# Performance work log

Hardware: AMD Instinct MI355X
Metric: run time of the kernel (lower is better)

The kernel has to match this reference:

```python
import jax, jax.numpy as jnp
import numpy as np

D_MODEL, D_QKV, N_HEADS = 1024, 64, 16


def setup_inputs() -> dict:
    key = jax.random.key(0)
    k_x, k_qkv, k_out = jax.random.split(key, 3)
    X = jax.random.normal(k_x, (2, 2048, D_MODEL), dtype=jnp.float32)
    # nn.Linear(d_model, 3*d_qkv*n_heads, bias=False): store as (in, out) for X @ W
    W_qkv = jax.random.normal(k_qkv, (D_MODEL, 3 * D_QKV * N_HEADS), dtype=jnp.float32) * (D_MODEL ** -0.5)
    W_out = jax.random.normal(k_out, (D_QKV * N_HEADS, D_MODEL), dtype=jnp.float32) * ((D_QKV * N_HEADS) ** -0.5)
    return {"X": X, "W_qkv": W_qkv, "W_out": W_out}


def reference(X, W_qkv, W_out):
    b, s, _ = X.shape
    h, d = N_HEADS, D_QKV
    scale = d ** 0.5
    qkv = X @ W_qkv                          # [b, s, 3*h*d]
    # Faithful to torch: view(b, s, h, d, 3).unbind(-1) -> interleaved q/k/v layout
    qkv = qkv.reshape(b, s, h, d, 3)
    q, k, v = qkv[..., 0], qkv[..., 1], qkv[..., 2]   # each [b, s, h, d]
    scores = jnp.einsum("bqhd,bkhd->bhqk", q, k) / scale
    weights = jax.nn.softmax(scores, axis=-1)          # [b, h, s, s]
    attn = jnp.einsum("bhqk,bkhd->bqhd", weights, v)   # [b, s, h, d]
    return attn.reshape(b, s, h * d) @ W_out           # [b, s, d_model]
```

## Files before the change

### kernel.cpp

```cpp
#include <hip/hip_runtime.h>
#include <hip/hip_bf16.h>
#include <math.h>

typedef __bf16 bf16;
typedef __bf16 bf16x2 __attribute__((ext_vector_type(2)));
typedef __bf16 bf16x4 __attribute__((ext_vector_type(4)));
typedef __bf16 bf16x8 __attribute__((ext_vector_type(8)));
typedef float f32x4 __attribute__((ext_vector_type(4)));
typedef float f32x16 __attribute__((ext_vector_type(16)));
typedef int i32x2 __attribute__((ext_vector_type(2)));
typedef int i32x4 __attribute__((ext_vector_type(4)));

#define MFMA16(a, b, c) __builtin_amdgcn_mfma_f32_16x16x32_bf16(a, b, c, 0, 0, 0)
#define MFMA32(a, b, c) __builtin_amdgcn_mfma_f32_32x32x16_bf16(a, b, c, 0, 0, 0)

constexpr int D_MODEL = 1024;
constexpr int N_QKV   = 3072;
constexpr int BATCH   = 2;
constexpr int SEQ     = 2048;
constexpr int NH      = 16;
constexpr int DH      = 64;
constexpr int M_TOT   = BATCH * SEQ;

__device__ __forceinline__ void gl_lds16(const bf16* g, bf16* l) {
    __builtin_amdgcn_global_load_lds(
        (const __attribute__((address_space(1))) void*)g,
        (__attribute__((address_space(3))) void*)l, 16, 0, 0);
}

__device__ __forceinline__ void pl32swap(int& a, int& b) {
    i32x2 r = __builtin_amdgcn_permlane32_swap(a, b, false, false);
    a = r[0];
    b = r[1];
}

template <int N> __device__ __forceinline__ void waitv() {
    asm volatile("s_waitcnt vmcnt(%0)" :: "n"(N) : "memory");
}
__device__ __forceinline__ void waitlgkm0() {
    asm volatile("s_waitcnt lgkmcnt(0)" ::: "memory");
}

__device__ __forceinline__ void transpose_tile(
    const float* __restrict__ in, bf16* __restrict__ out,
    int K, int N, int n0, int k0, bf16 (*T)[72], bool permute)
{
    const int tid = threadIdx.x;
    const int r   = tid >> 2;
    const int c4  = (tid & 3) * 16;

    const float* src = in + (size_t)(k0 + r) * N + n0 + c4;
    f32x4 v0 = *(const f32x4*)(src + 0);
    f32x4 v1 = *(const f32x4*)(src + 4);
    f32x4 v2 = *(const f32x4*)(src + 8);
    f32x4 v3 = *(const f32x4*)(src + 12);
    #pragma unroll
    for (int j = 0; j < 4; j++) {
        T[c4 + j][r]      = (bf16)v0[j];
        T[c4 + 4 + j][r]  = (bf16)v1[j];
        T[c4 + 8 + j][r]  = (bf16)v2[j];
        T[c4 + 12 + j][r] = (bf16)v3[j];
    }
    __syncthreads();
    int rowg = n0 + r;
    if (permute) {
        const int which = rowg % 3;
        const int h     = rowg / 192;
        const int d     = (rowg % 192) / 3;
        rowg = which * 1024 + h * 64 + d;
    }
    bf16* dst = out + (size_t)rowg * K + k0 + c4;
    *(bf16x8*)(dst)     = *(const bf16x8*)&T[r][c4];
    *(bf16x8*)(dst + 8) = *(const bf16x8*)&T[r][c4 + 8];
}

__global__ __launch_bounds__(256) void prepass_kernel(
    const float* __restrict__ X, const float* __restrict__ Wqkv,
    const float* __restrict__ Wout,
    bf16* __restrict__ xb, bf16* __restrict__ wqkv_t, bf16* __restrict__ wout_t)
{
    __shared__ bf16 T[64][72];
    const int b = blockIdx.x;
    if (b < 2048) {
        const size_t i = ((size_t)b * 256 + threadIdx.x) * 8;
        f32x4 a0 = *(const f32x4*)(X + i);
        f32x4 a1 = *(const f32x4*)(X + i + 4);
        bf16x8 w;
        #pragma unroll
        for (int j = 0; j < 4; j++) { w[j] = (bf16)a0[j]; w[j + 4] = (bf16)a1[j]; }
        *(bf16x8*)(xb + i) = w;
    } else if (b < 2048 + 768) {
        const int idx = b - 2048;
        transpose_tile(Wqkv, wqkv_t, D_MODEL, N_QKV,
                       (idx % 48) * 64, (idx / 48) * 64, T, true);
    } else {
        const int idx = b - 2816;
        transpose_tile(Wout, wout_t, D_MODEL, D_MODEL,
                       (idx % 16) * 64, (idx / 16) * 64, T, false);
    }
}

__global__ __launch_bounds__(512, 2) void qkv_gemm_kernel(
    const bf16* __restrict__ Xb, const bf16* __restrict__ Wt,
    bf16* __restrict__ qb, bf16* __restrict__ kb, bf16* __restrict__ vb)
{
    __shared__ __align__(16) bf16 smem[65536];
    bf16* const sA = smem;
    bf16* const sB = smem + 32768;

    const int tid  = threadIdx.x;
    const int wave = tid >> 6;
    const int lane = tid & 63;
    const int quad = lane >> 4;
    const int l16  = lane & 15;
    const int wr   = wave >> 2;
    const int wc   = wave & 3;
    const int m0   = blockIdx.x * 256;
    const int n0   = blockIdx.y * 256;

    const int sr2  = tid >> 3;
    const int c8p  = (tid & 7) ^ (sr2 & 7);
    const int stR0 = (sr2 << 1) | (c8p >> 2);
    const int stC0 = (c8p & 3) << 3;

    const bf16* Asrc = Xb + (size_t)(m0 + stR0) * D_MODEL + stC0;
    const bf16* Bsrc = Wt + (size_t)(n0 + stR0) * D_MODEL + stC0;

#define STG(s, kbo)                                                          \
    do {                                                                     \
        gl_lds16(Asrc + (kbo),                 sA + (s) * 8192 + tid * 8);   \
        gl_lds16(Asrc + 128 * D_MODEL + (kbo), sA + (s) * 8192 + 4096 + tid * 8); \
        gl_lds16(Bsrc + (kbo),                 sB + (s) * 8192 + tid * 8);   \
        gl_lds16(Bsrc + 128 * D_MODEL + (kbo), sB + (s) * 8192 + 4096 + tid * 8); \
    } while (0)

    const int foff = ((l16 >> 1) << 6) +
                     (((((l16 & 1) << 2) | quad) ^ ((l16 >> 1) & 7)) << 3);

    f32x4 acc[8][4];
    #pragma unroll
    for (int a = 0; a < 8; a++)
        #pragma unroll
        for (int b = 0; b < 4; b++) acc[a][b] = {0.f, 0.f, 0.f, 0.f};

#define PHASE(s, jn, DOSTG, WV)                                              \
    {                                                                        \
        const bf16* Ab_ = sA + (s) * 8192 + wr * 4096;                       \
        const bf16* Bb_ = sB + (s) * 8192 + wc * 2048;                       \
        bf16x8 af[8], bfr[4];                                                \
        _Pragma("unroll") for (int mi = 0; mi < 8; mi++)                     \
            af[mi] = *(const bf16x8*)&Ab_[mi * 512 + foff];                  \
        _Pragma("unroll") for (int ni = 0; ni < 4; ni++)                     \
            bfr[ni] = *(const bf16x8*)&Bb_[ni * 512 + foff];                 \
        waitlgkm0();                                                         \
        __builtin_amdgcn_s_barrier();                                        \
        if (DOSTG) { STG((s), (jn) * 32); }                                  \
        __builtin_amdgcn_s_setprio(1);                                       \
        _Pragma("unroll") for (int mi = 0; mi < 8; mi++)                     \
            _Pragma("unroll") for (int ni = 0; ni < 4; ni++)                 \
                acc[mi][ni] = MFMA16(af[mi], bfr[ni], acc[mi][ni]);          \
        __builtin_amdgcn_s_setprio(0);                                       \
        waitv<WV>();                                                         \
        __builtin_amdgcn_s_barrier();                                        \
    }

    STG(0, 0); STG(1, 32); STG(2, 64); STG(3, 96);
    waitv<12>();
    __builtin_amdgcn_s_barrier();

    for (int t = 0; t < 7; ++t) {
        const int j = t * 4;
        PHASE(0, j + 4, true, 12)
        PHASE(1, j + 5, true, 12)
        PHASE(2, j + 6, true, 12)
        PHASE(3, j + 7, true, 12)
    }
    PHASE(0, 0, false, 8)
    PHASE(1, 0, false, 4)
    PHASE(2, 0, false, 0)
    PHASE(3, 0, false, 0)

#undef PHASE
#undef STG

    const int bb     = m0 >> 11;
    const int s_base = m0 & (SEQ - 1);

    if (n0 < 2048) {
        bf16* dst0 = (n0 < 1024) ? qb : kb;
        const int h = ((n0 + wc * 64) >> 6) & 15;
        const size_t bh = (size_t)(bb * NH + h);
        #pragma unroll
        for (int mi = 0; mi < 8; mi++) {
            const int s0 = s_base + wr * 128 + mi * 16 + quad * 4;
            #pragma unroll
            for (int ni = 0; ni < 4; ni++) {
                const int d = ni * 16 + l16;
                #pragma unroll
                for (int i = 0; i < 4; i++)
                    dst0[(bh * SEQ + s0 + i) * DH + d] = (bf16)acc[mi][ni][i];
            }
        }
    } else {
        __syncthreads();
        bf16* T = smem;
        #pragma unroll
        for (int ni = 0; ni < 4; ni++) {
            const int nl = wc * 64 + ni * 16 + l16;
            #pragma unroll
            for (int mi = 0; mi < 8; mi++) {
                const int ml = wr * 128 + mi * 16 + quad * 4;
                bf16x4 pv;
                #pragma unroll
                for (int i = 0; i < 4; i++) pv[i] = (bf16)acc[mi][ni][i];
                const int c   = ml >> 3;
                const int swz = (c & 24) | ((c ^ nl) & 7);
                *(bf16x4*)&T[nl * 256 + swz * 8 + (ml & 7)] = pv;
            }
        }
        __syncthreads();
        const int hbase = (n0 - 2048) >> 6;
        #pragma unroll
        for (int it = 0; it < 8; it++) {
            const int nl = (tid >> 4) + it * 32;
            const int h  = hbase + (nl >> 6);
            const int d  = nl & 63;
            const size_t obase = ((size_t)(bb * NH + h) * DH + d) * SEQ + s_base;
            #pragma unroll
            for (int cc = 0; cc < 2; cc++) {
                const int c   = (tid & 15) + cc * 16;
                const int swz = (c & 24) | ((c ^ nl) & 7);
                bf16x8 vv = *(const bf16x8*)&T[nl * 256 + swz * 8];
                *(bf16x8*)(vb + obase + c * 8) = vv;
            }
        }
    }
}

__global__ __launch_bounds__(512, 4) void attn_kernel(
    const bf16* __restrict__ qb, const bf16* __restrict__ kb,
    const bf16* __restrict__ vb, bf16* __restrict__ ob)
{
    __shared__ __align__(16) bf16 smem[32768];

    const int tid  = threadIdx.x;
    const int wave = tid >> 6;
    const int grp  = wave >> 2;
    const int wq   = wave & 3;
    const int lane = tid & 63;
    const int l32  = lane & 31;
    const int hi   = lane >> 5;
    const int ltid = tid & 255;
    const int bh   = blockIdx.x;
    const int q0   = blockIdx.y * 128;
    const size_t base  = (size_t)bh * SEQ * DH;
    const int    kbase = grp * (SEQ / 2);

    bf16* const KsB = smem + grp * 2 * 4096;
    bf16* const VtB = smem + 16384 + grp * 2 * 4096;

    constexpr float QSCALE = 0.125f * 1.44269504f;

    bf16x8 qf[4];
    {
        const size_t qoff = base + (size_t)(q0 + wq * 32 + l32) * DH + hi * 8;
        #pragma unroll
        for (int kc = 0; kc < 4; kc++) {
            qf[kc] = *(const bf16x8*)(qb + qoff + kc * 16);
            #pragma unroll
            for (int j = 0; j < 8; j++)
                qf[kc][j] = (bf16)((float)qf[kc][j] * QSCALE);
        }
    }

    f32x16 o_acc[2];
    #pragma unroll
    for (int i = 0; i < 16; i++) { o_acc[0][i] = 0.f; o_acc[1][i] = 0.f; }
    float l_acc = 0.f;

    const int so0 = ltid;
    const int so1 = 256 + ltid;
    const int sr0 = so0 >> 3, sc0 = ((so0 & 7) ^ (sr0 & 7)) * 8;
    const int sr1 = so1 >> 3, sc1 = ((so1 & 7) ^ (sr1 & 7)) * 8;

    #define STAGE(bufi, kk0)                                                   \
        do {                                                                   \
            gl_lds16(kb + base + (size_t)(kbase + (kk0) + sr0) * DH + sc0,     \
                     KsB + (bufi) * 4096 + so0 * 8);                           \
            gl_lds16(kb + base + (size_t)(kbase + (kk0) + sr1) * DH + sc1,     \
                     KsB + (bufi) * 4096 + so1 * 8);                           \
            gl_lds16(vb + base + (size_t)sr0 * SEQ + kbase + (kk0) + sc0,      \
                     VtB + (bufi) * 4096 + so0 * 8);                           \
            gl_lds16(vb + base + (size_t)sr1 * SEQ + kbase + (kk0) + sc1,      \
                     VtB + (bufi) * 4096 + so1 * 8);                           \
        } while (0)

    STAGE(0, 0);
    int buf = 0;

    for (int kt = 0; kt < SEQ / 128; ++kt) {
        __syncthreads();
        if (kt + 1 < SEQ / 128) STAGE(buf ^ 1, (kt + 1) * 64);

        const bf16* Kst = KsB + buf * 4096;
        const bf16* Vtt = VtB + buf * 4096;

        #pragma unroll
        for (int kblk = 0; kblk < 2; kblk++) {
            f32x16 sacc;
            #pragma unroll
            for (int i = 0; i < 16; i++) sacc[i] = 0.f;
            #pragma unroll
            for (int kc = 0; kc < 4; kc++) {
                const int cko = ((2 * kc + hi) ^ (l32 & 7)) * 8;
                bf16x8 kf = *(const bf16x8*)
                    &Kst[(kblk * 32 + l32) * 64 + cko];
                sacc = MFMA32(kf, qf[kc], sacc);
            }

            int w[8];
            #pragma unroll
            for (int c = 0; c < 8; c++) {
                const float e0 = __builtin_amdgcn_exp2f(sacc[2 * c]);
                const float e1 = __builtin_amdgcn_exp2f(sacc[2 * c + 1]);
                l_acc += e0;
                l_acc += e1;
                bf16x2 t; t[0] = (bf16)e0; t[1] = (bf16)e1;
                w[c] = __builtin_bit_cast(int, t);
            }
            #pragma unroll
            for (int cc = 0; cc < 2; cc++) {
                pl32swap(w[cc * 4 + 0], w[cc * 4 + 2]);
                pl32swap(w[cc * 4 + 1], w[cc * 4 + 3]);
                i32x4 fi = {w[cc * 4 + 0], w[cc * 4 + 1],
                            w[cc * 4 + 2], w[cc * 4 + 3]};
                bf16x8 pa = __builtin_bit_cast(bf16x8, fi);

                const int kc = kblk * 2 + cc;
                const int cko = ((2 * kc + hi) ^ (l32 & 7)) * 8;
                #pragma unroll
                for (int nb = 0; nb < 2; nb++) {
                    bf16x8 vf = *(const bf16x8*)
                        &Vtt[(nb * 32 + l32) * 64 + cko];
                    o_acc[nb] = MFMA32(pa, vf, o_acc[nb]);
                }
            }
        }
        buf ^= 1;
    }
    #undef STAGE

    const float l_q = l_acc + __shfl_xor(l_acc, 32);

    float* cO  = (float*)smem;
    float* cL1 = (float*)smem + 8192;
    float* cL2 = (float*)smem + 8320;

    __syncthreads();
    if (grp == 1) {
        #pragma unroll
        for (int nb = 0; nb < 2; nb++)
            #pragma unroll
            for (int c4 = 0; c4 < 4; c4++) {
                const int j = nb * 4 + c4;
                f32x4 v = { o_acc[nb][c4 * 4 + 0], o_acc[nb][c4 * 4 + 1],
                            o_acc[nb][c4 * 4 + 2], o_acc[nb][c4 * 4 + 3] };
                *(f32x4*)&cO[(wq * 64 + lane) * 32 + ((j ^ (lane & 7)) * 4)] = v;
            }
        if (hi == 0) cL1[wq * 32 + l32] = l_q;
    }
    __syncthreads();
    if (grp == 0) {
        #pragma unroll
        for (int nb = 0; nb < 2; nb++)
            #pragma unroll
            for (int c4 = 0; c4 < 4; c4++) {
                const int j = nb * 4 + c4;
                f32x4 v = *(const f32x4*)
                    &cO[(wq * 64 + lane) * 32 + ((j ^ (lane & 7)) * 4)];
                #pragma unroll
                for (int e = 0; e < 4; e++) o_acc[nb][c4 * 4 + e] += v[e];
            }
        if (hi == 0) cL2[wq * 32 + l32] = l_q + cL1[wq * 32 + l32];
    }
    __syncthreads();
    if (grp == 0) {
        const int b = bh >> 4, h = bh & 15;
        #pragma unroll
        for (int i = 0; i < 16; i++) {
            const int qrow = (i & 3) + 8 * (i >> 2) + 4 * hi;
            const int q = q0 + wq * 32 + qrow;
            const float li = 1.0f / cL2[wq * 32 + qrow];
            #pragma unroll
            for (int nb = 0; nb < 2; nb++)
                ob[((size_t)(b * SEQ + q) * NH + h) * DH + nb * 32 + l32] =
                    (bf16)(o_acc[nb][i] * li);
        }
    }
}

__global__ __launch_bounds__(256) void out_gemm_kernel(
    const bf16* __restrict__ A, const bf16* __restrict__ Wt,
    float* __restrict__ out)
{
    __shared__ __align__(16) bf16 As[128 * 64];
    __shared__ __align__(16) bf16 Bs[128 * 64];

    const int tid  = threadIdx.x;
    const int wave = tid >> 6;
    const int lane = tid & 63;
    const int quad = lane >> 4;
    const int l16  = lane & 15;
    const int sw   = l16 & 7;
    const int m0   = blockIdx.x * 128;
    const int n0   = blockIdx.y * 128;
    const int wm   = (wave & 1) * 64;
    const int wn   = (wave >> 1) * 64;

    const int srow = lane >> 3;
    const int sc_s = ((lane & 7) ^ srow) * 8;
    const int sc_d = (lane & 7) * 8;

    f32x4 acc[4][4];
    #pragma unroll
    for (int a = 0; a < 4; a++)
        #pragma unroll
        for (int b = 0; b < 4; b++) acc[a][b] = {0.f, 0.f, 0.f, 0.f};

    for (int kb0 = 0; kb0 < D_MODEL; kb0 += 64) {
        __syncthreads();
        #pragma unroll
        for (int j = 0; j < 4; j++) {
            const int row = wave * 32 + j * 8 + srow;
            gl_lds16(A  + (size_t)(m0 + row) * D_MODEL + kb0 + sc_s,
                     As + row * 64 + sc_d);
            gl_lds16(Wt + (size_t)(n0 + row) * D_MODEL + kb0 + sc_s,
                     Bs + row * 64 + sc_d);
        }
        __syncthreads();

        #pragma unroll
        for (int ks = 0; ks < 2; ks++) {
            const int co = ((ks * 4 + quad) ^ sw) * 8;
            bf16x8 af[4], bfr[4];
            #pragma unroll
            for (int mi = 0; mi < 4; mi++)
                af[mi] = *(const bf16x8*)&As[(wm + mi * 16 + l16) * 64 + co];
            #pragma unroll
            for (int ni = 0; ni < 4; ni++)
                bfr[ni] = *(const bf16x8*)&Bs[(wn + ni * 16 + l16) * 64 + co];
            #pragma unroll
            for (int mi = 0; mi < 4; mi++)
                #pragma unroll
                for (int ni = 0; ni < 4; ni++)
                    acc[mi][ni] = MFMA16(af[mi], bfr[ni], acc[mi][ni]);
        }
    }

    #pragma unroll
    for (int mi = 0; mi < 4; mi++) {
        const int row0 = m0 + wm + mi * 16 + quad * 4;
        #pragma unroll
        for (int ni = 0; ni < 4; ni++) {
            const int n = n0 + wn + ni * 16 + l16;
            #pragma unroll
            for (int i = 0; i < 4; i++)
                out[(size_t)(row0 + i) * D_MODEL + n] = acc[mi][ni][i];
        }
    }
}

extern "C" void kernel_launch(void* const* d_in, const int* in_sizes, int n_in,
                              void* d_out, int out_size, void* d_ws, size_t ws_size,
                              hipStream_t stream)
{
    const float* X    = (const float*)d_in[0];
    const float* Wqkv = (const float*)d_in[1];
    const float* Wout = (const float*)d_in[2];
    float* out        = (float*)d_out;

    const size_t n_elem = (size_t)M_TOT * D_MODEL;
    bf16* qb      = (bf16*)d_ws;
    bf16* kb      = qb + n_elem;
    bf16* vb      = kb + n_elem;
    bf16* attnb   = vb + n_elem;
    bf16* wqkv_t  = attnb + n_elem;
    bf16* wout_t  = wqkv_t + (size_t)N_QKV * D_MODEL;
    bf16* xb      = wout_t + (size_t)D_MODEL * D_MODEL;

    prepass_kernel<<<3072, 256, 0, stream>>>(X, Wqkv, Wout, xb, wqkv_t, wout_t);

    qkv_gemm_kernel<<<dim3(M_TOT / 256, N_QKV / 256), 512, 0, stream>>>(
        xb, wqkv_t, qb, kb, vb);
    attn_kernel<<<dim3(BATCH * NH, SEQ / 128), 512, 0, stream>>>(qb, kb, vb, attnb);
    out_gemm_kernel<<<dim3(M_TOT / 128, D_MODEL / 128), 256, 0, stream>>>(
        attnb, wout_t, out);
}
```

Measured before the change: 176.7 us.

## Pipeline out-projection GEMM with 4-stage LDS ring and compute row sums via MFMA

The output-projection GEMM is rebuilt around a four-stage LDS ring buffer with k-chunks of 32. Loads are issued asynchronously ahead of compute, fenced by explicit waitcnt and barrier calls, with raised wave priority around the MFMAs, so global-load latency overlaps with matrix math instead of sitting behind two syncthreads per iteration. In the attention kernel the softmax denominator is now accumulated by an extra MFMA against a vector of ones instead of scalar adds. This removes the per-element adds and one reduction barrier, but the sum is taken over bf16-rounded weights, which changes numerics slightly. The GEMM adds launch_bounds(256,2) and doubles its shared memory to 64KB.

```diff
diff --git a/kernel.cpp b/kernel.cpp
--- a/kernel.cpp
+++ b/kernel.cpp
@@ -273,10 +273,16 @@
         }
     }
 
+    bf16x8 ones;
+    #pragma unroll
+    for (int j = 0; j < 8; j++) ones[j] = (bf16)1.0f;
+
     f32x16 o_acc[2];
+    f32x16 o_l;
     #pragma unroll
-    for (int i = 0; i < 16; i++) { o_acc[0][i] = 0.f; o_acc[1][i] = 0.f; }
-    float l_acc = 0.f;
+    for (int i = 0; i < 16; i++) {
+        o_acc[0][i] = 0.f; o_acc[1][i] = 0.f; o_l[i] = 0.f;
+    }
 
     const int so0 = ltid;
     const int so1 = 256 + ltid;
@@ -321,11 +327,9 @@
             int w[8];
             #pragma unroll
             for (int c = 0; c < 8; c++) {
-                const float e0 = __builtin_amdgcn_exp2f(sacc[2 * c]);
-                const float e1 = __builtin_amdgcn_exp2f(sacc[2 * c + 1]);
-                l_acc += e0;
-                l_acc += e1;
-                bf16x2 t; t[0] = (bf16)e0; t[1] = (bf16)e1;
+                bf16x2 t;
+                t[0] = (bf16)__builtin_amdgcn_exp2f(sacc[2 * c]);
+                t[1] = (bf16)__builtin_amdgcn_exp2f(sacc[2 * c + 1]);
                 w[c] = __builtin_bit_cast(int, t);
             }
             #pragma unroll
@@ -338,6 +342,7 @@
 
                 const int kc = kblk * 2 + cc;
                 const int cko = ((2 * kc + hi) ^ (l32 & 7)) * 8;
+                o_l = MFMA32(pa, ones, o_l);
                 #pragma unroll
                 for (int nb = 0; nb < 2; nb++) {
                     bf16x8 vf = *(const bf16x8*)
@@ -350,11 +355,8 @@
     }
     #undef STAGE
 
-    const float l_q = l_acc + __shfl_xor(l_acc, 32);
-
     float* cO  = (float*)smem;
     float* cL1 = (float*)smem + 8192;
-    float* cL2 = (float*)smem + 8320;
 
     __syncthreads();
     if (grp == 1) {
@@ -367,7 +369,11 @@
                             o_acc[nb][c4 * 4 + 2], o_acc[nb][c4 * 4 + 3] };
                 *(f32x4*)&cO[(wq * 64 + lane) * 32 + ((j ^ (lane & 7)) * 4)] = v;
             }
-        if (hi == 0) cL1[wq * 32 + l32] = l_q;
+        if (l32 == 0) {
+            #pragma unroll
+            for (int i = 0; i < 16; i++)
+                cL1[wq * 32 + ((i & 3) + 8 * (i >> 2) + 4 * hi)] = o_l[i];
+        }
     }
     __syncthreads();
     if (grp == 0) {
@@ -381,16 +387,12 @@
                 #pragma unroll
                 for (int e = 0; e < 4; e++) o_acc[nb][c4 * 4 + e] += v[e];
             }
-        if (hi == 0) cL2[wq * 32 + l32] = l_q + cL1[wq * 32 + l32];
-    }
-    __syncthreads();
-    if (grp == 0) {
         const int b = bh >> 4, h = bh & 15;
         #pragma unroll
         for (int i = 0; i < 16; i++) {
             const int qrow = (i & 3) + 8 * (i >> 2) + 4 * hi;
             const int q = q0 + wq * 32 + qrow;
-            const float li = 1.0f / cL2[wq * 32 + qrow];
+            const float li = 1.0f / (o_l[i] + cL1[wq * 32 + qrow]);
             #pragma unroll
             for (int nb = 0; nb < 2; nb++)
                 ob[((size_t)(b * SEQ + q) * NH + h) * DH + nb * 32 + l32] =
@@ -399,27 +401,42 @@
     }
 }
 
-__global__ __launch_bounds__(256) void out_gemm_kernel(
+__global__ __launch_bounds__(256, 2) void out_gemm_kernel(
     const bf16* __restrict__ A, const bf16* __restrict__ Wt,
     float* __restrict__ out)
 {
-    __shared__ __align__(16) bf16 As[128 * 64];
-    __shared__ __align__(16) bf16 Bs[128 * 64];
+    __shared__ __align__(16) bf16 smem[32768];
+    bf16* const sA = smem;
+    bf16* const sB = smem + 16384;
 
     const int tid  = threadIdx.x;
     const int wave = tid >> 6;
     const int lane = tid & 63;
     const int quad = lane >> 4;
     const int l16  = lane & 15;
-    const int sw   = l16 & 7;
+    const int wr   = wave >> 1;
+    const int wc   = wave & 1;
     const int m0   = blockIdx.x * 128;
     const int n0   = blockIdx.y * 128;
-    const int wm   = (wave & 1) * 64;
-    const int wn   = (wave >> 1) * 64;
-
-    const int srow = lane >> 3;
-    const int sc_s = ((lane & 7) ^ srow) * 8;
-    const int sc_d = (lane & 7) * 8;
+
+    const int sr2  = tid >> 3;
+    const int c8p  = (tid & 7) ^ (sr2 & 7);
+    const int stR0 = (sr2 << 1) | (c8p >> 2);
+    const int stC0 = (c8p & 3) << 3;
+
+    const bf16* Asrc = A  + (size_t)(m0 + stR0) * D_MODEL + stC0;
+    const bf16* Bsrc = Wt + (size_t)(n0 + stR0) * D_MODEL + stC0;
+
+#define STG(s, kbo)                                                          \
+    do {                                                                     \
+        gl_lds16(Asrc + (kbo),                sA + (s) * 4096 + tid * 8);    \
+        gl_lds16(Asrc + 64 * D_MODEL + (kbo), sA + (s) * 4096 + 2048 + tid * 8); \
+        gl_lds16(Bsrc + (kbo),                sB + (s) * 4096 + tid * 8);    \
+        gl_lds16(Bsrc + 64 * D_MODEL + (kbo), sB + (s) * 4096 + 2048 + tid * 8); \
+    } while (0)
+
+    const int foff = ((l16 >> 1) << 6) +
+                     (((((l16 & 1) << 2) | quad) ^ ((l16 >> 1) & 7)) << 3);
 
     f32x4 acc[4][4];
     #pragma unroll
@@ -427,42 +444,52 @@
         #pragma unroll
         for (int b = 0; b < 4; b++) acc[a][b] = {0.f, 0.f, 0.f, 0.f};
 
-    for (int kb0 = 0; kb0 < D_MODEL; kb0 += 64) {
-        __syncthreads();
-        #pragma unroll
-        for (int j = 0; j < 4; j++) {
-            const int row = wave * 32 + j * 8 + srow;
-            gl_lds16(A  + (size_t)(m0 + row) * D_MODEL + kb0 + sc_s,
-                     As + row * 64 + sc_d);
-            gl_lds16(Wt + (size_t)(n0 + row) * D_MODEL + kb0 + sc_s,
-                     Bs + row * 64 + sc_d);
-        }
-        __syncthreads();
-
-        #pragma unroll
-        for (int ks = 0; ks < 2; ks++) {
-            const int co = ((ks * 4 + quad) ^ sw) * 8;
-            bf16x8 af[4], bfr[4];
-            #pragma unroll
-            for (int mi = 0; mi < 4; mi++)
-                af[mi] = *(const bf16x8*)&As[(wm + mi * 16 + l16) * 64 + co];
-            #pragma unroll
-            for (int ni = 0; ni < 4; ni++)
-                bfr[ni] = *(const bf16x8*)&Bs[(wn + ni * 16 + l16) * 64 + co];
-            #pragma unroll
-            for (int mi = 0; mi < 4; mi++)
-                #pragma unroll
-                for (int ni = 0; ni < 4; ni++)
-                    acc[mi][ni] = MFMA16(af[mi], bfr[ni], acc[mi][ni]);
-        }
-    }
+#define PHASE(s, jn, DOSTG, WV)                                              \
+    {                                                                        \
+        const bf16* Ab_ = sA + (s) * 4096 + wr * 2048;                       \
+        const bf16* Bb_ = sB + (s) * 4096 + wc * 2048;                       \
+        bf16x8 af[4], bfr[4];                                                \
+        _Pragma("unroll") for (int mi = 0; mi < 4; mi++)                     \
+            af[mi] = *(const bf16x8*)&Ab_[mi * 512 + foff];                  \
+        _Pragma("unroll") for (int ni = 0; ni < 4; ni++)                     \
+            bfr[ni] = *(const bf16x8*)&Bb_[ni * 512 + foff];                 \
+        waitlgkm0();                                                         \
+        __builtin_amdgcn_s_barrier();                                        \
+        if (DOSTG) { STG((s), (jn) * 32); }                                  \
+        __builtin_amdgcn_s_setprio(1);                                       \
+        _Pragma("unroll") for (int mi = 0; mi < 4; mi++)                     \
+            _Pragma("unroll") for (int ni = 0; ni < 4; ni++)                 \
+                acc[mi][ni] = MFMA16(af[mi], bfr[ni], acc[mi][ni]);          \
+        __builtin_amdgcn_s_setprio(0);                                       \
+        waitv<WV>();                                                         \
+        __builtin_amdgcn_s_barrier();                                        \
+    }
+
+    STG(0, 0); STG(1, 32); STG(2, 64); STG(3, 96);
+    waitv<12>();
+    __builtin_amdgcn_s_barrier();
+
+    for (int t = 0; t < 7; ++t) {
+        const int j = t * 4;
+        PHASE(0, j + 4, true, 12)
+        PHASE(1, j + 5, true, 12)
+        PHASE(2, j + 6, true, 12)
+        PHASE(3, j + 7, true, 12)
+    }
+    PHASE(0, 0, false, 8)
+    PHASE(1, 0, false, 4)
+    PHASE(2, 0, false, 0)
+    PHASE(3, 0, false, 0)
+
+#undef PHASE
+#undef STG
 
     #pragma unroll
     for (int mi = 0; mi < 4; mi++) {
-        const int row0 = m0 + wm + mi * 16 + quad * 4;
+        const int row0 = m0 + wr * 64 + mi * 16 + quad * 4;
         #pragma unroll
         for (int ni = 0; ni < 4; ni++) {
-            const int n = n0 + wn + ni * 16 + l16;
+            const int n = n0 + wc * 64 + ni * 16 + l16;
             #pragma unroll
             for (int i = 0; i < 4; i++)
                 out[(size_t)(row0 + i) * D_MODEL + n] = acc[mi][ni][i];
```

Result: faster. 170.2 us (-3.6%).
